# Kernel tuning notes

Measured on AMD Instinct MI355X. Metric: run time of the kernel, lower is better.

The kernel has to match this reference:

```python
import jax, jax.numpy as jnp
import numpy as np

TEMPERATURE = 1.0
N_NODES = 50000
N_EDGES = 1600000
BATCH = 2
C_IN = 64
C_OUT = 64


def setup_inputs() -> dict:
    key = jax.random.key(0)
    k = jax.random.split(key, 8)
    # edge_index with no self-loops: tgt = (src + 1 + off) % N, off in [0, N-2)
    src = jax.random.randint(k[0], (N_EDGES,), 0, N_NODES, dtype=jnp.int64)
    off = jax.random.randint(k[1], (N_EDGES,), 0, N_NODES - 1, dtype=jnp.int64)
    tgt = (src + 1 + off) % N_NODES
    edge_index = jnp.stack([src, tgt])  # (2, E)
    x = jax.random.normal(k[2], (BATCH, N_NODES, C_IN), dtype=jnp.float32)
    f_disc_orig = jax.random.uniform(k[3], (N_EDGES,), dtype=jnp.float32)
    fluxes = jax.random.normal(k[4], (BATCH, N_NODES), dtype=jnp.float32)
    W_conc = jax.random.normal(k[5], (C_OUT, C_IN), dtype=jnp.float32) * (1.0 / np.sqrt(C_IN))
    W_disc = jax.random.normal(k[6], (C_OUT, C_IN), dtype=jnp.float32) * (1.0 / np.sqrt(C_IN))
    bias = jnp.zeros((C_OUT,), dtype=jnp.float32)
    return {"x": x, "edge_index": edge_index, "f_disc_orig": f_disc_orig,
            "fluxes": fluxes, "W_conc": W_conc, "W_disc": W_disc, "bias": bias}


def reference(x, edge_index, f_disc_orig, fluxes, W_conc, W_disc, bias):
    B, N, _ = x.shape
    src0, tgt0 = edge_index[0], edge_index[1]  # original edges (no self-loops)
    loops = jnp.arange(N, dtype=edge_index.dtype)
    src = jnp.concatenate([src0, loops])  # (E+N,)
    tgt = jnp.concatenate([tgt0, loops])
    # GCN symmetric normalization D^{-1/2} A D^{-1/2} (with self-loops)
    deg = jnp.zeros((N,), x.dtype).at[tgt].add(1.0)
    dis = jnp.where(deg > 0, jax.lax.rsqrt(jnp.maximum(deg, 1e-30)), 0.0)
    norm = dis[src] * dis[tgt]  # (E+N,)
    # dynamic discordant strength on original (non-self-loop) edges
    sign_prod = jnp.tanh(fluxes[:, src0] * fluxes[:, tgt0] / TEMPERATURE)  # (B, E)
    keep = (1.0 + sign_prod) * 0.5
    fdo = f_disc_orig[None, :]
    f_disc = keep * fdo + (1.0 - keep) * (1.0 - fdo)  # (B, E)
    # self-loop messages are purely concordant (f_disc = 0)
    f_full = jnp.concatenate([f_disc, jnp.zeros((B, N), x.dtype)], axis=1)  # (B, E+N)
    # transform once per node, then gather per edge
    xc = jnp.einsum('bni,oi->bno', x, W_conc)  # (B, N, O)
    xd = jnp.einsum('bni,oi->bno', x, W_disc)
    msg = norm[None, :, None] * ((1.0 - f_full)[..., None] * xc[:, src] +
                                 f_full[..., None] * xd[:, src])  # (B, E+N, O)
    out = jnp.zeros((B, N, xc.shape[-1]), x.dtype).at[:, tgt].add(msg)
    return out + bias
```

## Files before the change

kernel.cpp:

```cpp
#include <hip/hip_runtime.h>
#include <math.h>


constexpr int C = 64;
constexpr int CNB = 128;
constexpr int CCAP = 5120;

typedef short short8 __attribute__((ext_vector_type(8)));
typedef float f32x4 __attribute__((ext_vector_type(4)));

__device__ __forceinline__ unsigned pack_bf16x2(float a, float b) {
    unsigned ua = __float_as_uint(a);
    ua = (ua + 0x7fffu + ((ua >> 16) & 1u)) >> 16;
    unsigned ub = __float_as_uint(b);
    ub = (ub + 0x7fffu + ((ub >> 16) & 1u)) >> 16;
    return ua | (ub << 16);
}
__device__ __forceinline__ float bflo(unsigned p) { return __uint_as_float(p << 16); }
__device__ __forceinline__ float bfhi(unsigned p) { return __uint_as_float(p & 0xffff0000u); }

__global__ __launch_bounds__(256) void convert_kernel(
    const float* __restrict__ x, unsigned* __restrict__ xb2, int nwords,
    int* __restrict__ coarseCursor, int ncoarse) {
    int i = blockIdx.x * blockDim.x + threadIdx.x;
    if (i < ncoarse) coarseCursor[i] = 0;
    int stride = gridDim.x * blockDim.x;
    const float2* x2 = (const float2*)x;
    for (int w = i; w < nwords; w += stride) {
        float2 xv = x2[w];
        xb2[w] = pack_bf16x2(xv.x, xv.y);
    }
}

__global__ __launch_bounds__(256) void binA1_kernel(
    const int* __restrict__ src, const int* __restrict__ tgt,
    const float* __restrict__ fdo, int* __restrict__ coarseCursor,
    unsigned long long* __restrict__ slab, int E, int ncoarse) {
    __shared__ int hcnt[512];
    __shared__ int hbase[512];
    const int tid = threadIdx.x;
    const int chunk0 = blockIdx.x * 8192;
    for (int c = tid; c < 512; c += 256) hcnt[c] = 0;
    __syncthreads();
#pragma unroll 4
    for (int k = 0; k < 32; ++k) {
        int e = chunk0 + tid + k * 256;
        if (e < E) atomicAdd(&hcnt[tgt[e] >> 7], 1);
    }
    __syncthreads();
    for (int c = tid; c < ncoarse; c += 256) {
        int cc = hcnt[c];
        hbase[c] = cc ? atomicAdd(&coarseCursor[c], cc) : 0;
        hcnt[c] = 0;
    }
    __syncthreads();
#pragma unroll 4
    for (int k = 0; k < 32; ++k) {
        int e = chunk0 + tid + k * 256;
        if (e < E) {
            int t = tgt[e];
            int b = t >> 7;
            int pos = hbase[b] + atomicAdd(&hcnt[b], 1);
            if (pos < CCAP) {
                unsigned q = (unsigned)(fdo[e] * 32767.0f + 0.5f);
                unsigned long long en = (unsigned long long)(unsigned)src[e]
                                      | ((unsigned long long)(unsigned)(t & 127) << 17)
                                      | ((unsigned long long)q << 24);
                slab[(size_t)b * CCAP + pos] = en;
            }
        }
    }
}

__global__ __launch_bounds__(1024) void binA2_kernel(
    const unsigned long long* __restrict__ slab,
    const int* __restrict__ coarseCursor, const float* __restrict__ flux,
    unsigned* __restrict__ epackFine, float4* __restrict__ nodeinfo, int N) {
    const int b = blockIdx.x;
    const int tid = threadIdx.x;
    __shared__ int ncnt[CNB];
    __shared__ int nsc[CNB];
    __shared__ int ncur[CNB];
    int cnt = min(coarseCursor[b], CCAP);
    if (tid < CNB) { ncnt[tid] = 0; ncur[tid] = 0; }
    __syncthreads();
    const unsigned long long* sl = slab + (size_t)b * CCAP;
    for (int i = tid; i < cnt; i += 1024)
        atomicAdd(&ncnt[(int)((sl[i] >> 17) & 127)], 1);
    __syncthreads();
    if (tid < CNB) nsc[tid] = ncnt[tid];
    __syncthreads();
    for (int off = 1; off < CNB; off <<= 1) {
        int v = (tid < CNB && tid >= off) ? nsc[tid - off] : 0;
        __syncthreads();
        if (tid < CNB) nsc[tid] += v;
        __syncthreads();
    }
    for (int i = tid; i < cnt; i += 1024) {
        unsigned long long e = sl[i];
        int s = (int)(e & 0x1FFFFull);
        int tl = (int)((e >> 17) & 127);
        unsigned q = (unsigned)((e >> 24) & 0x7FFF);
        int pos = nsc[tl] - ncnt[tl] + atomicAdd(&ncur[tl], 1);
        epackFine[(size_t)b * CCAP + pos] = (unsigned)s | (q << 17);
    }
    if (tid < CNB) {
        int n = b * CNB + tid;
        if (n < N) {
            int dg = ncnt[tid];
            int rs = b * CCAP + (nsc[tid] - dg);
            float4 ni;
            ni.x = rsqrtf((float)(dg + 1));
            ni.y = flux[n];
            ni.z = flux[N + n];
            ni.w = __int_as_float((dg << 21) | rs);
            nodeinfo[n] = ni;
        }
    }
}

__global__ __launch_bounds__(256) void aggregate_kernel(
    const float4* __restrict__ nodeinfo, const unsigned* __restrict__ epackFine,
    const unsigned* __restrict__ xb2, unsigned* __restrict__ up,
    unsigned* __restrict__ vp, int N) {
    const int lane = threadIdx.x & 63;
    const int wslot = threadIdx.x >> 6;
    const int node = blockIdx.x * 4 + wslot;
    __shared__ float4 s_e[4][2][64];
    if (node >= N) return;
    const int e2 = lane >> 4;
    const int q16 = lane & 15;
    const int g = q16 >> 3;
    const int p = q16 & 7;
    float4 ni = nodeinfo[node];
    const unsigned wbits = (unsigned)__float_as_int(ni.w);
    const int start = (int)(wbits & 0x1FFFFFu);
    const int end = start + (int)(wbits >> 21);
    const float dt = ni.x, f0t = ni.y, f1t = ni.z;
    const char* xbg = (const char*)xb2 + (size_t)g * N * 128 + p * 16;
    float au[8] = {0, 0, 0, 0, 0, 0, 0, 0};
    float av[8] = {0, 0, 0, 0, 0, 0, 0, 0};
    for (int base = start; base < end; base += 64) {
        int cnt = min(64, end - base);
        int cntp = (cnt + 3) & ~3;
        if (lane < cnt) {
            unsigned pe = epackFine[base + lane];
            int s = (int)(pe & 0x1FFFFu);
            float fd = (float)(pe >> 17) * (1.0f / 32767.0f);
            float4 nis = nodeinfo[s];
            float nrm = nis.x * dt;
            float p0 = nis.y * f0t;
            float p1 = nis.z * f1t;
            float k0 = 1.0f / (1.0f + __expf(-2.0f * p0));
            float k1 = 1.0f / (1.0f + __expf(-2.0f * p1));
            float w = 2.0f * fd - 1.0f;
            float f0 = fmaf(k0, w, 1.0f - fd);
            float f1 = fmaf(k1, w, 1.0f - fd);
            float soff = __int_as_float(s << 7);
            s_e[wslot][0][lane] = make_float4(soff, nrm * (1.0f - f0), nrm * f0, 0.f);
            s_e[wslot][1][lane] = make_float4(soff, nrm * (1.0f - f1), nrm * f1, 0.f);
        } else if (lane < cntp) {
            float4 z = make_float4(0.f, 0.f, 0.f, 0.f);
            s_e[wslot][0][lane] = z;
            s_e[wslot][1][lane] = z;
        }
        float4 r0 = s_e[wslot][g][e2];
        uint4 xwN = *(const uint4*)(xbg + __float_as_int(r0.x));
        float ccN = r0.y, cdN = r0.z;
        for (int j = 4; j < cntp; j += 4) {
            uint4 xw = xwN;
            float cc = ccN, cd = cdN;
            float4 r2 = s_e[wslot][g][j + e2];
            xwN = *(const uint4*)(xbg + __float_as_int(r2.x));
            ccN = r2.y; cdN = r2.z;
#pragma unroll
            for (int w = 0; w < 4; ++w) {
                unsigned xp = (&xw.x)[w];
                float lo = bflo(xp), hi = bfhi(xp);
                au[2 * w] = fmaf(cc, lo, au[2 * w]);
                au[2 * w + 1] = fmaf(cc, hi, au[2 * w + 1]);
                av[2 * w] = fmaf(cd, lo, av[2 * w]);
                av[2 * w + 1] = fmaf(cd, hi, av[2 * w + 1]);
            }
        }
#pragma unroll
        for (int w = 0; w < 4; ++w) {
            unsigned xp = (&xwN.x)[w];
            float lo = bflo(xp), hi = bfhi(xp);
            au[2 * w] = fmaf(ccN, lo, au[2 * w]);
            au[2 * w + 1] = fmaf(ccN, hi, au[2 * w + 1]);
            av[2 * w] = fmaf(cdN, lo, av[2 * w]);
            av[2 * w + 1] = fmaf(cdN, hi, av[2 * w + 1]);
        }
    }
#pragma unroll
    for (int k = 0; k < 8; ++k) {
        au[k] += __shfl_xor(au[k], 16, 64);
        au[k] += __shfl_xor(au[k], 32, 64);
        av[k] += __shfl_xor(av[k], 16, 64);
        av[k] += __shfl_xor(av[k], 32, 64);
    }
    if (e2 == 0) {
        uint4 xs = *(const uint4*)(xbg + ((size_t)node << 7));
        float d2 = dt * dt;
#pragma unroll
        for (int w = 0; w < 4; ++w) {
            unsigned xp = (&xs.x)[w];
            au[2 * w] = fmaf(d2, bflo(xp), au[2 * w]);
            au[2 * w + 1] = fmaf(d2, bfhi(xp), au[2 * w + 1]);
        }
        uint4 uo, vo;
        uo.x = pack_bf16x2(au[0], au[1]);
        uo.y = pack_bf16x2(au[2], au[3]);
        uo.z = pack_bf16x2(au[4], au[5]);
        uo.w = pack_bf16x2(au[6], au[7]);
        vo.x = pack_bf16x2(av[0], av[1]);
        vo.y = pack_bf16x2(av[2], av[3]);
        vo.z = pack_bf16x2(av[4], av[5]);
        vo.w = pack_bf16x2(av[6], av[7]);
        size_t wo = ((size_t)(g * N + node)) * 32 + 4 * p;
        *(uint4*)(up + wo) = uo;
        *(uint4*)(vp + wo) = vo;
    }
}

__device__ __forceinline__ short8 make_bfrag(const float* __restrict__ row, int off) {
    const float4* p = (const float4*)(row + off);
    float4 lo = p[0], hi = p[1];
    uint4 w;
    w.x = pack_bf16x2(lo.x, lo.y);
    w.y = pack_bf16x2(lo.z, lo.w);
    w.z = pack_bf16x2(hi.x, hi.y);
    w.w = pack_bf16x2(hi.z, hi.w);
    return __builtin_bit_cast(short8, w);
}

__global__ __launch_bounds__(256) void gemm_mfma_kernel(
    const unsigned* __restrict__ up, const unsigned* __restrict__ vp,
    const float* __restrict__ Wc, const float* __restrict__ Wd,
    const float* __restrict__ bias, float* __restrict__ out, int ntiles) {
    const int lane = threadIdx.x & 63;
    const int nl = lane & 15;
    const int quad = lane >> 4;
    const int wave = blockIdx.x * 4 + (threadIdx.x >> 6);
    const int nwaves = gridDim.x * 4;

    short8 bf[4][4];
    float bt[4];
#pragma unroll
    for (int t = 0; t < 4; ++t) {
        int n = 16 * t + nl;
        const float* wcr = Wc + n * 64;
        const float* wdr = Wd + n * 64;
        bf[0][t] = make_bfrag(wcr, quad * 8);
        bf[1][t] = make_bfrag(wcr, 32 + quad * 8);
        bf[2][t] = make_bfrag(wdr, quad * 8);
        bf[3][t] = make_bfrag(wdr, 32 + quad * 8);
        bt[t] = bias[n];
    }

    for (int tile = wave; tile < ntiles; tile += nwaves) {
        int row = tile * 16 + nl;
        const uint4* ur = (const uint4*)(up + (size_t)row * 32);
        const uint4* vr = (const uint4*)(vp + (size_t)row * 32);
        short8 a0 = __builtin_bit_cast(short8, ur[quad]);
        short8 a1 = __builtin_bit_cast(short8, ur[4 + quad]);
        short8 a2 = __builtin_bit_cast(short8, vr[quad]);
        short8 a3 = __builtin_bit_cast(short8, vr[4 + quad]);
        f32x4 acc[4];
#pragma unroll
        for (int t = 0; t < 4; ++t) {
            f32x4 z = {0.f, 0.f, 0.f, 0.f};
            acc[t] = __builtin_amdgcn_mfma_f32_16x16x32_bf16(a0, bf[0][t], z, 0, 0, 0);
            acc[t] = __builtin_amdgcn_mfma_f32_16x16x32_bf16(a1, bf[1][t], acc[t], 0, 0, 0);
            acc[t] = __builtin_amdgcn_mfma_f32_16x16x32_bf16(a2, bf[2][t], acc[t], 0, 0, 0);
            acc[t] = __builtin_amdgcn_mfma_f32_16x16x32_bf16(a3, bf[3][t], acc[t], 0, 0, 0);
        }
        float* ob = out + ((size_t)(tile * 16 + quad * 4) << 6);
#pragma unroll
        for (int t = 0; t < 4; ++t) {
            int col = 16 * t + nl;
#pragma unroll
            for (int r = 0; r < 4; ++r)
                ob[(r << 6) + col] = acc[t][r] + bt[t];
        }
    }
}

extern "C" void kernel_launch(void* const* d_in, const int* in_sizes, int n_in,
                              void* d_out, int out_size, void* d_ws, size_t ws_size,
                              hipStream_t stream) {
    const float* x = (const float*)d_in[0];
    const int* ei = (const int*)d_in[1];
    const float* fdo = (const float*)d_in[2];
    const float* flux = (const float*)d_in[3];
    const float* Wc = (const float*)d_in[4];
    const float* Wd = (const float*)d_in[5];
    const float* bias = (const float*)d_in[6];
    float* out = (float*)d_out;

    const int E = in_sizes[2];
    const int BN = in_sizes[3];
    const int N = BN / 2;
    const int ncoarse = (N + CNB - 1) / CNB;

    auto align = [](size_t o) { return (o + 255) & ~(size_t)255; };
    char* ws = (char*)d_ws;
    size_t o = 0;
    int* coarseCursor = (int*)(ws + o);            o = align(o + (size_t)ncoarse * 4);
    float4* nodeinfo = (float4*)(ws + o);          o = align(o + (size_t)N * 16);
    unsigned long long* slab = (unsigned long long*)(ws + o);
    unsigned* up = (unsigned*)slab;
    o = align(o + (size_t)ncoarse * CCAP * 8);
    unsigned* epackFine = (unsigned*)(ws + o);     o = align(o + (size_t)ncoarse * CCAP * 4);
    unsigned* xb2 = (unsigned*)(ws + o);           o = align(o + (size_t)BN * 32 * 4);
    unsigned* vp = (unsigned*)(ws + o);            o += (size_t)BN * 32 * 4;

    const int* srcp = ei;
    const int* tgtp = ei + E;

    convert_kernel<<<2048, 256, 0, stream>>>(x, xb2, BN * 32, coarseCursor, ncoarse);
    binA1_kernel<<<(E + 8191) / 8192, 256, 0, stream>>>(srcp, tgtp, fdo,
                                                        coarseCursor, slab, E, ncoarse);
    binA2_kernel<<<ncoarse, 1024, 0, stream>>>(slab, coarseCursor, flux,
                                               epackFine, nodeinfo, N);
    aggregate_kernel<<<(N + 3) / 4, 256, 0, stream>>>(nodeinfo, epackFine, xb2,
                                                      up, vp, N);
    gemm_mfma_kernel<<<512, 256, 0, stream>>>(up, vp, Wc, Wd, bias, out, BN / 16);
}
```

Measured before the change: 225.3 us.

## Replace two-level coarse binning with global degree count, scan, and atomic scatter

Swaps the hierarchical CSR build (coarse bins via a shared-memory histogram into a slab, then per-bin fine sorting) for a flat pipeline: global atomic degree count, a per-block scan chained through an atomic base counter, and an atomic-cursor scatter into a compact edge array. This drops the 8-byte slab round trip and the fixed-capacity CCAP padding, but adds global atomics per edge on random targets (two passes) and one extra kernel launch. Row order across scan blocks now follows atomic order and is no longer monotone by node, which may hurt locality in aggregation.

```diff
diff --git a/kernel.cpp b/kernel.cpp
--- a/kernel.cpp
+++ b/kernel.cpp
@@ -3,8 +3,6 @@
 
 
 constexpr int C = 64;
-constexpr int CNB = 128;
-constexpr int CCAP = 5120;
 
 typedef short short8 __attribute__((ext_vector_type(8)));
 typedef float f32x4 __attribute__((ext_vector_type(4)));
@@ -21,9 +19,9 @@
 
 __global__ __launch_bounds__(256) void convert_kernel(
     const float* __restrict__ x, unsigned* __restrict__ xb2, int nwords,
-    int* __restrict__ coarseCursor, int ncoarse) {
+    int* __restrict__ degc, int N) {
     int i = blockIdx.x * blockDim.x + threadIdx.x;
-    if (i < ncoarse) coarseCursor[i] = 0;
+    if (i <= N) degc[i] = 0;
     int stride = gridDim.x * blockDim.x;
     const float2* x2 = (const float2*)x;
     for (int w = i; w < nwords; w += stride) {
@@ -32,90 +30,54 @@
     }
 }
 
-__global__ __launch_bounds__(256) void binA1_kernel(
+__global__ __launch_bounds__(256) void degcount_kernel(
+    const int* __restrict__ tgt, int* __restrict__ degc, int E) {
+    int i = blockIdx.x * blockDim.x + threadIdx.x;
+    int stride = gridDim.x * blockDim.x;
+    for (int e = i; e < E; e += stride) atomicAdd(&degc[tgt[e]], 1);
+}
+
+__global__ __launch_bounds__(256) void scan_kernel(
+    int* __restrict__ degc, const float* __restrict__ flux,
+    float4* __restrict__ nodeinfo, int N) {
+    __shared__ int sc[256];
+    __shared__ int sbase;
+    const int tid = threadIdx.x;
+    const int n = blockIdx.x * 256 + tid;
+    int dg = (n < N) ? degc[n] : 0;
+    sc[tid] = dg;
+    __syncthreads();
+    for (int off = 1; off < 256; off <<= 1) {
+        int v = (tid >= off) ? sc[tid - off] : 0;
+        __syncthreads();
+        sc[tid] += v;
+        __syncthreads();
+    }
+    if (tid == 255) sbase = atomicAdd(&degc[N], sc[255]);
+    __syncthreads();
+    if (n < N) {
+        int rs = sbase + sc[tid] - dg;
+        degc[n] = rs;
+        float4 ni;
+        ni.x = rsqrtf((float)(dg + 1));
+        ni.y = flux[n];
+        ni.z = flux[N + n];
+        ni.w = __int_as_float((dg << 21) | rs);
+        nodeinfo[n] = ni;
+    }
+}
+
+__global__ __launch_bounds__(256) void scatter_kernel(
     const int* __restrict__ src, const int* __restrict__ tgt,
-    const float* __restrict__ fdo, int* __restrict__ coarseCursor,
-    unsigned long long* __restrict__ slab, int E, int ncoarse) {
-    __shared__ int hcnt[512];
-    __shared__ int hbase[512];
-    const int tid = threadIdx.x;
-    const int chunk0 = blockIdx.x * 8192;
-    for (int c = tid; c < 512; c += 256) hcnt[c] = 0;
-    __syncthreads();
-#pragma unroll 4
-    for (int k = 0; k < 32; ++k) {
-        int e = chunk0 + tid + k * 256;
-        if (e < E) atomicAdd(&hcnt[tgt[e] >> 7], 1);
-    }
-    __syncthreads();
-    for (int c = tid; c < ncoarse; c += 256) {
-        int cc = hcnt[c];
-        hbase[c] = cc ? atomicAdd(&coarseCursor[c], cc) : 0;
-        hcnt[c] = 0;
-    }
-    __syncthreads();
-#pragma unroll 4
-    for (int k = 0; k < 32; ++k) {
-        int e = chunk0 + tid + k * 256;
-        if (e < E) {
-            int t = tgt[e];
-            int b = t >> 7;
-            int pos = hbase[b] + atomicAdd(&hcnt[b], 1);
-            if (pos < CCAP) {
-                unsigned q = (unsigned)(fdo[e] * 32767.0f + 0.5f);
-                unsigned long long en = (unsigned long long)(unsigned)src[e]
-                                      | ((unsigned long long)(unsigned)(t & 127) << 17)
-                                      | ((unsigned long long)q << 24);
-                slab[(size_t)b * CCAP + pos] = en;
-            }
-        }
-    }
-}
-
-__global__ __launch_bounds__(1024) void binA2_kernel(
-    const unsigned long long* __restrict__ slab,
-    const int* __restrict__ coarseCursor, const float* __restrict__ flux,
-    unsigned* __restrict__ epackFine, float4* __restrict__ nodeinfo, int N) {
-    const int b = blockIdx.x;
-    const int tid = threadIdx.x;
-    __shared__ int ncnt[CNB];
-    __shared__ int nsc[CNB];
-    __shared__ int ncur[CNB];
-    int cnt = min(coarseCursor[b], CCAP);
-    if (tid < CNB) { ncnt[tid] = 0; ncur[tid] = 0; }
-    __syncthreads();
-    const unsigned long long* sl = slab + (size_t)b * CCAP;
-    for (int i = tid; i < cnt; i += 1024)
-        atomicAdd(&ncnt[(int)((sl[i] >> 17) & 127)], 1);
-    __syncthreads();
-    if (tid < CNB) nsc[tid] = ncnt[tid];
-    __syncthreads();
-    for (int off = 1; off < CNB; off <<= 1) {
-        int v = (tid < CNB && tid >= off) ? nsc[tid - off] : 0;
-        __syncthreads();
-        if (tid < CNB) nsc[tid] += v;
-        __syncthreads();
-    }
-    for (int i = tid; i < cnt; i += 1024) {
-        unsigned long long e = sl[i];
-        int s = (int)(e & 0x1FFFFull);
-        int tl = (int)((e >> 17) & 127);
-        unsigned q = (unsigned)((e >> 24) & 0x7FFF);
-        int pos = nsc[tl] - ncnt[tl] + atomicAdd(&ncur[tl], 1);
-        epackFine[(size_t)b * CCAP + pos] = (unsigned)s | (q << 17);
-    }
-    if (tid < CNB) {
-        int n = b * CNB + tid;
-        if (n < N) {
-            int dg = ncnt[tid];
-            int rs = b * CCAP + (nsc[tid] - dg);
-            float4 ni;
-            ni.x = rsqrtf((float)(dg + 1));
-            ni.y = flux[n];
-            ni.z = flux[N + n];
-            ni.w = __int_as_float((dg << 21) | rs);
-            nodeinfo[n] = ni;
-        }
+    const float* __restrict__ fdo, int* __restrict__ cursors,
+    unsigned* __restrict__ epack, int E) {
+    int i = blockIdx.x * blockDim.x + threadIdx.x;
+    int stride = gridDim.x * blockDim.x;
+    for (int e = i; e < E; e += stride) {
+        int t = tgt[e];
+        int pos = atomicAdd(&cursors[t], 1);
+        unsigned q = (unsigned)(fdo[e] * 32767.0f + 0.5f);
+        epack[pos] = (unsigned)src[e] | (q << 17);
     }
 }
 
@@ -302,29 +264,25 @@
     const int E = in_sizes[2];
     const int BN = in_sizes[3];
     const int N = BN / 2;
-    const int ncoarse = (N + CNB - 1) / CNB;
 
     auto align = [](size_t o) { return (o + 255) & ~(size_t)255; };
     char* ws = (char*)d_ws;
     size_t o = 0;
-    int* coarseCursor = (int*)(ws + o);            o = align(o + (size_t)ncoarse * 4);
+    int* degc = (int*)(ws + o);                    o = align(o + (size_t)(N + 1) * 4);
     float4* nodeinfo = (float4*)(ws + o);          o = align(o + (size_t)N * 16);
-    unsigned long long* slab = (unsigned long long*)(ws + o);
-    unsigned* up = (unsigned*)slab;
-    o = align(o + (size_t)ncoarse * CCAP * 8);
-    unsigned* epackFine = (unsigned*)(ws + o);     o = align(o + (size_t)ncoarse * CCAP * 4);
+    unsigned* epack = (unsigned*)(ws + o);         o = align(o + (size_t)E * 4);
     unsigned* xb2 = (unsigned*)(ws + o);           o = align(o + (size_t)BN * 32 * 4);
+    unsigned* up = (unsigned*)(ws + o);            o = align(o + (size_t)BN * 32 * 4);
     unsigned* vp = (unsigned*)(ws + o);            o += (size_t)BN * 32 * 4;
 
     const int* srcp = ei;
     const int* tgtp = ei + E;
 
-    convert_kernel<<<2048, 256, 0, stream>>>(x, xb2, BN * 32, coarseCursor, ncoarse);
-    binA1_kernel<<<(E + 8191) / 8192, 256, 0, stream>>>(srcp, tgtp, fdo,
-                                                        coarseCursor, slab, E, ncoarse);
-    binA2_kernel<<<ncoarse, 1024, 0, stream>>>(slab, coarseCursor, flux,
-                                               epackFine, nodeinfo, N);
-    aggregate_kernel<<<(N + 3) / 4, 256, 0, stream>>>(nodeinfo, epackFine, xb2,
+    convert_kernel<<<2048, 256, 0, stream>>>(x, xb2, BN * 32, degc, N);
+    degcount_kernel<<<2048, 256, 0, stream>>>(tgtp, degc, E);
+    scan_kernel<<<(N + 255) / 256, 256, 0, stream>>>(degc, flux, nodeinfo, N);
+    scatter_kernel<<<2048, 256, 0, stream>>>(srcp, tgtp, fdo, degc, epack, E);
+    aggregate_kernel<<<(N + 3) / 4, 256, 0, stream>>>(nodeinfo, epack, xb2,
                                                       up, vp, N);
     gemm_mfma_kernel<<<512, 256, 0, stream>>>(up, vp, Wc, Wd, bias, out, BN / 16);
 }
```

After: 361.3 us. +60.4%, slower.
